# Performance work log

Hardware: AMD Instinct MI355X
Metric: run time of the kernel (lower is better)

Reference implementation:

```python
import jax, jax.numpy as jnp
import numpy as np

B, M, HID = 4, 4096, 1024
H, HD = 16, 64          # num_heads, head_dim
SEG = 128               # segment_size
DIL = 2                 # dilation_rate
SCALE = HD ** -0.5


def _hilbert_perm(n_side):
    """Linear indices (y*n+x) visited along a Hilbert curve on an n_side x n_side grid."""
    def d2xy(n, d):
        x = y = 0
        t = d
        s = 1
        while s < n:
            rx = 1 & (t // 2)
            ry = 1 & (t ^ rx)
            if ry == 0:
                if rx == 1:
                    x = s - 1 - x
                    y = s - 1 - y
                x, y = y, x
            x += s * rx
            y += s * ry
            t //= 4
            s *= 2
        return x, y
    idx = np.empty(n_side * n_side, dtype=np.int32)
    for d in range(n_side * n_side):
        x, y = d2xy(n_side, d)
        idx[d] = y * n_side + x
    return idx


def setup_inputs() -> dict:
    key = jax.random.key(0)
    k1, k2, k3 = jax.random.split(key, 3)
    x = jax.random.normal(k1, (B, M, HID), dtype=jnp.float32)
    w_qkv = jax.random.normal(k2, (3 * HID, HID), dtype=jnp.float32) * 0.02
    w_out = jax.random.normal(k3, (HID, HID), dtype=jnp.float32) * 0.02
    hilbert_map = jnp.asarray(_hilbert_perm(int(np.sqrt(M))))  # permutation of [0, M)
    return {"x": x, "w_qkv": w_qkv, "w_out": w_out, "hilbert_map": hilbert_map}


def reference(x, w_qkv, w_out, hilbert_map):
    nseg = M // SEG
    # qkv projection (nn.Linear, no bias): [B, M, 3*HID]
    qkv = x @ w_qkv.T
    qkv = qkv.reshape(B, M, 3, H, HD).transpose(2, 0, 3, 1, 4)  # [3, B, H, M, HD]
    # Hilbert reorder along sequence dim
    qkv = qkv[:, :, :, hilbert_map, :]
    q, k, v = qkv[0], qkv[1], qkv[2]
    # segment into blocks of SEG: [B, H, nseg, SEG, HD]
    q = q.reshape(B, H, nseg, SEG, HD)
    k = k.reshape(B, H, nseg, SEG, HD)
    v = v.reshape(B, H, nseg, SEG, HD)
    scores = jnp.einsum("bhnsd,bhntd->bhnst", q, k) * SCALE
    # dilation mask: position is active if (pos % DIL == 0); pair allowed if row OR col active
    active = (jnp.arange(SEG) % DIL) == 0
    mask = active[:, None] | active[None, :]  # [SEG, SEG]
    scores = jnp.where(mask, scores, jnp.float32(-1e30))
    attn = jax.nn.softmax(scores, axis=-1)
    out = jnp.einsum("bhnst,bhntd->bhnsd", attn, v)  # [B, H, nseg, SEG, HD]
    # output stays in Hilbert order (matches custom autograd semantics)
    out = out.reshape(B, H, M, HD).transpose(0, 2, 1, 3).reshape(B, M, HID)
    return out @ w_out.T
```

## Files before the change

kernel.cpp:

```cpp
#include <hip/hip_runtime.h>
#include <stdint.h>


typedef __attribute__((ext_vector_type(8))) short short8;
typedef __attribute__((ext_vector_type(4))) short short4v;
typedef __attribute__((ext_vector_type(4))) float f32x4;

#define DEV __device__ __forceinline__

DEV short f2bf(float f) {
  union { float f; uint32_t u; } x; x.f = f;
  uint32_t r = x.u + 0x7fffu + ((x.u >> 16) & 1u);
  return (short)(r >> 16);
}

DEV void gload_lds16(const void* g, void* l) {
  __builtin_amdgcn_global_load_lds(
      (const __attribute__((address_space(1))) uint32_t*)g,
      (__attribute__((address_space(3))) uint32_t*)l, 16, 0, 0);
}

__global__ __launch_bounds__(256) void k_gather_cast(
    const float* __restrict__ x, const int* __restrict__ perm, short* __restrict__ xp) {
  const int row = blockIdx.x;
  const int b = row >> 12, pos = row & 4095;
  const int src = (b << 12) + perm[pos];
  const f32x4 v = ((const f32x4*)(x + (size_t)src * 1024))[threadIdx.x];
  short4v o = { f2bf(v[0]), f2bf(v[1]), f2bf(v[2]), f2bf(v[3]) };
  ((short4v*)(xp + (size_t)row * 1024))[threadIdx.x] = o;
}

__global__ __launch_bounds__(256) void k_cast(
    const float* __restrict__ src, short* __restrict__ dst) {
  const int i = blockIdx.x * 256 + threadIdx.x;
  const f32x4 v = ((const f32x4*)src)[i];
  short4v o = { f2bf(v[0]), f2bf(v[1]), f2bf(v[2]), f2bf(v[3]) };
  ((short4v*)dst)[i] = o;
}

template <int EPI>
__global__ __launch_bounds__(256, 3) void k_gemm(
    const short* __restrict__ A, const short* __restrict__ W,
    void* __restrict__ Cout, const int K, const int N) {
  __shared__ __attribute__((aligned(16))) short As[128 * 64];
  __shared__ __attribute__((aligned(16))) short Bs[128 * 64];
  const int tid = threadIdx.x;
  const int bi = blockIdx.y, bj = blockIdx.x;
  const int lane = tid & 63, w = tid >> 6;
  const int wr = w >> 1, wc = w & 1;
  const int lrow = lane & 15, lg = lane >> 4;

  f32x4 acc[4][4] = {};
  const size_t arow0 = (size_t)bi * 128;
  const size_t brow0 = (size_t)bj * 128;

  for (int k0 = 0; k0 < K; k0 += 64) {
    __syncthreads();
#pragma unroll
    for (int i = 0; i < 4; ++i) {
      int c = i * 256 + tid;
      int row = c >> 3, ch = c & 7;
      int g = ch ^ (row & 7);
      gload_lds16(A + (arow0 + row) * K + k0 + g * 8, &As[c * 8]);
      gload_lds16(W + (brow0 + row) * K + k0 + g * 8, &Bs[c * 8]);
    }
    __syncthreads();
#pragma unroll
    for (int kk = 0; kk < 2; ++kk) {
      short8 af[4], bfr[4];
#pragma unroll
      for (int mi = 0; mi < 4; ++mi) {
        int r = wr * 64 + mi * 16 + lrow;
        int pc = (kk * 4 + lg) ^ (r & 7);
        af[mi] = *(const short8*)&As[r * 64 + pc * 8];
      }
#pragma unroll
      for (int ni = 0; ni < 4; ++ni) {
        int r = wc * 64 + ni * 16 + lrow;
        int pc = (kk * 4 + lg) ^ (r & 7);
        bfr[ni] = *(const short8*)&Bs[r * 64 + pc * 8];
      }
#pragma unroll
      for (int mi = 0; mi < 4; ++mi)
#pragma unroll
        for (int ni = 0; ni < 4; ++ni)
          acc[mi][ni] = __builtin_amdgcn_mfma_f32_16x16x32_bf16(
              af[mi], bfr[ni], acc[mi][ni], 0, 0, 0);
    }
  }

  const int gr_base = bi * 128 + wr * 64;
  const int gc_base = bj * 128 + wc * 64;
  if (EPI == 0) {
    short* Q = (short*)Cout;
#pragma unroll
    for (int mi = 0; mi < 4; ++mi) {
#pragma unroll
      for (int reg = 0; reg < 4; ++reg) {
        int gr = gr_base + mi * 16 + 4 * lg + reg;
        int b = gr >> 12, pos = gr & 4095;
#pragma unroll
        for (int ni = 0; ni < 4; ++ni) {
          int gc = gc_base + ni * 16 + lrow;
          int sel = gc >> 10, h = (gc >> 6) & 15, d = gc & 63;
          size_t idx = ((((size_t)sel * 4 + b) * 16 + h) * 4096 + pos) * 64 + d;
          Q[idx] = f2bf(acc[mi][ni][reg]);
        }
      }
    }
  } else {
    float* C = (float*)Cout;
#pragma unroll
    for (int mi = 0; mi < 4; ++mi)
#pragma unroll
      for (int reg = 0; reg < 4; ++reg) {
        int gr = gr_base + mi * 16 + 4 * lg + reg;
#pragma unroll
        for (int ni = 0; ni < 4; ++ni) {
          int gc = gc_base + ni * 16 + lrow;
          C[(size_t)gr * N + gc] = acc[mi][ni][reg];
        }
      }
  }
}

__global__ __launch_bounds__(256, 2) void k_attn(
    const short* __restrict__ qkv, short* __restrict__ aout) {
  __shared__ __attribute__((aligned(16))) short Qs[128 * 64];
  __shared__ __attribute__((aligned(16))) short Ks[128 * 64];
  __shared__ __attribute__((aligned(16))) short Vt[64 * 128];
  __shared__ __attribute__((aligned(16))) short Ps[128 * 128];
  const int bid = blockIdx.x;
  const int seg = bid & 31, h = (bid >> 5) & 15, b = bid >> 9;
  const size_t plane = (size_t)4096 * 64;
  const short* qp = qkv + ((size_t)(0 * 4 + b) * 16 + h) * plane + seg * 128 * 64;
  const short* kp = qkv + ((size_t)(1 * 4 + b) * 16 + h) * plane + seg * 128 * 64;
  const short* vp = qkv + ((size_t)(2 * 4 + b) * 16 + h) * plane + seg * 128 * 64;
  const int tid = threadIdx.x, lane = tid & 63, w = tid >> 6;
  const int lrow = lane & 15, lg = lane >> 4;

#pragma unroll
  for (int i = 0; i < 4; ++i) {
    int c = i * 256 + tid;
    int row = c >> 3, ch = c & 7, g = ch ^ (row & 7);
    gload_lds16(qp + row * 64 + g * 8, &Qs[c * 8]);
    gload_lds16(kp + row * 64 + g * 8, &Ks[c * 8]);
  }
#pragma unroll
  for (int i = 0; i < 4; ++i) {
    int c = i * 256 + tid;
    int t = c >> 3, d0 = (c & 7) * 8;
    short8 v = *(const short8*)(vp + t * 64 + d0);
#pragma unroll
    for (int j = 0; j < 8; ++j) {
      int d = d0 + j;
      Vt[d * 128 + (t ^ ((d & 7) * 8))] = v[j];
    }
  }
  __syncthreads();

  f32x4 s[2][8] = {};
#pragma unroll
  for (int kk = 0; kk < 2; ++kk) {
    short8 qa[2];
#pragma unroll
    for (int mi = 0; mi < 2; ++mi) {
      int r = w * 32 + mi * 16 + lrow;
      int pc = (kk * 4 + lg) ^ (r & 7);
      qa[mi] = *(const short8*)&Qs[r * 64 + pc * 8];
    }
#pragma unroll
    for (int ni = 0; ni < 8; ++ni) {
      int r = ni * 16 + lrow;
      int pc = (kk * 4 + lg) ^ (r & 7);
      short8 kb = *(const short8*)&Ks[r * 64 + pc * 8];
#pragma unroll
      for (int mi = 0; mi < 2; ++mi)
        s[mi][ni] = __builtin_amdgcn_mfma_f32_16x16x32_bf16(qa[mi], kb, s[mi][ni], 0, 0, 0);
    }
  }

  float inv[2][4];
  const int oddcol = lane & 1;
#pragma unroll
  for (int mi = 0; mi < 2; ++mi) {
#pragma unroll
    for (int reg = 0; reg < 4; ++reg) {
      float pm = -3.0e38f;
#pragma unroll
      for (int ni = 0; ni < 8; ++ni) {
        float v = s[mi][ni][reg] * 0.125f;
        if ((reg & 1) && oddcol) v = -1.0e30f;
        s[mi][ni][reg] = v;
        pm = fmaxf(pm, v);
      }
#pragma unroll
      for (int off = 1; off < 16; off <<= 1) pm = fmaxf(pm, __shfl_xor(pm, off));
      float sum = 0.f;
#pragma unroll
      for (int ni = 0; ni < 8; ++ni) {
        float p = __expf(s[mi][ni][reg] - pm);
        s[mi][ni][reg] = p;
        sum += p;
      }
#pragma unroll
      for (int off = 1; off < 16; off <<= 1) sum += __shfl_xor(sum, off);
      inv[mi][reg] = 1.0f / sum;
    }
  }

#pragma unroll
  for (int mi = 0; mi < 2; ++mi)
#pragma unroll
    for (int ni = 0; ni < 8; ++ni)
#pragma unroll
      for (int reg = 0; reg < 4; ++reg) {
        int r = w * 32 + mi * 16 + 4 * lg + reg;
        int col = ni * 16 + lrow;
        Ps[r * 128 + (col ^ ((r & 7) * 8))] = f2bf(s[mi][ni][reg]);
      }

  f32x4 o[2][4] = {};
#pragma unroll
  for (int kt = 0; kt < 4; ++kt) {
    short8 pa[2];
#pragma unroll
    for (int mi = 0; mi < 2; ++mi) {
      int r = w * 32 + mi * 16 + lrow;
      int pc = (kt * 4 + lg) ^ (r & 7);
      pa[mi] = *(const short8*)&Ps[r * 128 + pc * 8];
    }
#pragma unroll
    for (int dn = 0; dn < 4; ++dn) {
      int d = dn * 16 + lrow;
      int pc = (kt * 4 + lg) ^ (d & 7);
      short8 vb = *(const short8*)&Vt[d * 128 + pc * 8];
#pragma unroll
      for (int mi = 0; mi < 2; ++mi)
        o[mi][dn] = __builtin_amdgcn_mfma_f32_16x16x32_bf16(pa[mi], vb, o[mi][dn], 0, 0, 0);
    }
  }

#pragma unroll
  for (int mi = 0; mi < 2; ++mi)
#pragma unroll
    for (int dn = 0; dn < 4; ++dn)
#pragma unroll
      for (int reg = 0; reg < 4; ++reg) {
        int r = w * 32 + mi * 16 + 4 * lg + reg;
        int pos = seg * 128 + r;
        int d = dn * 16 + lrow;
        aout[((size_t)(b * 4096 + pos)) * 1024 + h * 64 + d] =
            f2bf(o[mi][dn][reg] * inv[mi][reg]);
      }
}

extern "C" void kernel_launch(void* const* d_in, const int* in_sizes, int n_in,
                              void* d_out, int out_size, void* d_ws, size_t ws_size,
                              hipStream_t stream) {
  const float* x     = (const float*)d_in[0];
  const float* w_qkv = (const float*)d_in[1];
  const float* w_out = (const float*)d_in[2];
  const int*   perm  = (const int*)d_in[3];

  char* ws = (char*)d_ws;
  short* xp   = (short*)(ws);
  short* wq   = (short*)(ws + 33554432);
  short* wo   = (short*)(ws + 33554432 + 6291456);
  short* qkvb = (short*)(ws + 41943040);
  short* aout = xp;

  k_gather_cast<<<16384, 256, 0, stream>>>(x, perm, xp);
  k_cast<<<3072, 256, 0, stream>>>(w_qkv, wq);
  k_cast<<<1024, 256, 0, stream>>>(w_out, wo);
  k_gemm<0><<<dim3(24, 128), 256, 0, stream>>>(xp, wq, qkvb, 1024, 3072);
  k_attn<<<2048, 256, 0, stream>>>(qkvb, aout);
  k_gemm<1><<<dim3(8, 128), 256, 0, stream>>>(aout, wo, d_out, 1024, 1024);
}
```

Before: 322.4 us.

## Rewrite GEMMs as 256x256 8-wave double-buffered pipelined kernels; alias attention LDS

```diff
diff --git a/kernel.cpp b/kernel.cpp
--- a/kernel.cpp
+++ b/kernel.cpp
@@ -19,6 +19,11 @@
       (const __attribute__((address_space(1))) uint32_t*)g,
       (__attribute__((address_space(3))) uint32_t*)l, 16, 0, 0);
 }
+
+#define BAR() __builtin_amdgcn_s_barrier()
+#define LGKM0() do { asm volatile("s_waitcnt lgkmcnt(0)" ::: "memory"); \
+                     __builtin_amdgcn_sched_barrier(0); } while (0)
+#define VMC(n) asm volatile("s_waitcnt vmcnt(" #n ")" ::: "memory")
 
 __global__ __launch_bounds__(256) void k_gather_cast(
     const float* __restrict__ x, const int* __restrict__ perm, short* __restrict__ xp) {
@@ -38,98 +43,143 @@
   ((short4v*)dst)[i] = o;
 }
 
-template <int EPI>
-__global__ __launch_bounds__(256, 3) void k_gemm(
-    const short* __restrict__ A, const short* __restrict__ W,
-    void* __restrict__ Cout, const int K, const int N) {
-  __shared__ __attribute__((aligned(16))) short As[128 * 64];
-  __shared__ __attribute__((aligned(16))) short Bs[128 * 64];
+template <int EPI, int NBJ>
+__global__ __launch_bounds__(512, 2) void k_gemm8(
+    const short* __restrict__ A, const short* __restrict__ W, void* __restrict__ Cout) {
+  __shared__ __attribute__((aligned(16))) short lds[65536];
   const int tid = threadIdx.x;
-  const int bi = blockIdx.y, bj = blockIdx.x;
   const int lane = tid & 63, w = tid >> 6;
-  const int wr = w >> 1, wc = w & 1;
+  const int wr = w >> 2, wc = w & 3;
   const int lrow = lane & 15, lg = lane >> 4;
 
-  f32x4 acc[4][4] = {};
-  const size_t arow0 = (size_t)bi * 128;
-  const size_t brow0 = (size_t)bj * 128;
-
-  for (int k0 = 0; k0 < K; k0 += 64) {
-    __syncthreads();
-#pragma unroll
-    for (int i = 0; i < 4; ++i) {
-      int c = i * 256 + tid;
-      int row = c >> 3, ch = c & 7;
-      int g = ch ^ (row & 7);
-      gload_lds16(A + (arow0 + row) * K + k0 + g * 8, &As[c * 8]);
-      gload_lds16(W + (brow0 + row) * K + k0 + g * 8, &Bs[c * 8]);
-    }
-    __syncthreads();
-#pragma unroll
-    for (int kk = 0; kk < 2; ++kk) {
-      short8 af[4], bfr[4];
-#pragma unroll
-      for (int mi = 0; mi < 4; ++mi) {
-        int r = wr * 64 + mi * 16 + lrow;
-        int pc = (kk * 4 + lg) ^ (r & 7);
-        af[mi] = *(const short8*)&As[r * 64 + pc * 8];
-      }
-#pragma unroll
-      for (int ni = 0; ni < 4; ++ni) {
-        int r = wc * 64 + ni * 16 + lrow;
-        int pc = (kk * 4 + lg) ^ (r & 7);
-        bfr[ni] = *(const short8*)&Bs[r * 64 + pc * 8];
-      }
-#pragma unroll
-      for (int mi = 0; mi < 4; ++mi)
-#pragma unroll
-        for (int ni = 0; ni < 4; ++ni)
-          acc[mi][ni] = __builtin_amdgcn_mfma_f32_16x16x32_bf16(
-              af[mi], bfr[ni], acc[mi][ni], 0, 0, 0);
-    }
-  }
-
-  const int gr_base = bi * 128 + wr * 64;
-  const int gc_base = bj * 128 + wc * 64;
+  const int nwg = NBJ * 64;
+  const int cpx = nwg >> 3;
+  const int bid = blockIdx.x;
+  const int sw = (bid & 7) * cpx + (bid >> 3);
+  const int bi = sw / NBJ, bj = sw % NBJ;
+
+  const short* Abase = A + (size_t)bi * 256 * 1024;
+  const short* Bbase = W + (size_t)bj * 256 * 1024;
+
+  const int c0 = tid, c1 = tid + 512;
+  const int sOff0 = (c0 >> 3) * 1024 + (((c0 & 7) ^ ((c0 >> 3) & 7)) * 8);
+  const int sOff1 = (c1 >> 3) * 1024 + (((c1 & 7) ^ ((c1 >> 3) & 7)) * 8);
+  const int pc0 = lg ^ (lrow & 7), pc1 = (4 + lg) ^ (lrow & 7);
+
+  f32x4 acc[2][4][2][2] = {};
+  short8 af[4][2], bfrag[2][2][2];
+
+#define ISSUE(base, half, tile, isB) do {                                   \
+    const short* _s = (base) + (half) * (128 * 1024) + (tile) * 64;         \
+    short* _d = lds + (((tile) & 1) * 32768) + (isB) * 16384 + (half) * 8192; \
+    gload_lds16(_s + sOff0, _d + c0 * 8);                                   \
+    gload_lds16(_s + sOff1, _d + c1 * 8);                                   \
+  } while (0)
+
+#define LDA(mh) do {                                                        \
+    const short* _b = ldsbuf + (mh) * 8192;                                 \
+    _Pragma("unroll") for (int mi = 0; mi < 4; ++mi) {                      \
+      const short* _r = _b + (wr * 64 + mi * 16 + lrow) * 64;               \
+      af[mi][0] = *(const short8*)(_r + pc0 * 8);                           \
+      af[mi][1] = *(const short8*)(_r + pc1 * 8); } } while (0)
+
+#define LDB(nh) do {                                                        \
+    const short* _b = ldsbuf + 16384 + (nh) * 8192;                         \
+    _Pragma("unroll") for (int ni = 0; ni < 2; ++ni) {                      \
+      const short* _r = _b + (wc * 32 + ni * 16 + lrow) * 64;               \
+      bfrag[nh][ni][0] = *(const short8*)(_r + pc0 * 8);                    \
+      bfrag[nh][ni][1] = *(const short8*)(_r + pc1 * 8); } } while (0)
+
+#define MM(mh, nh) do {                                                     \
+    _Pragma("unroll") for (int mi = 0; mi < 4; ++mi)                        \
+    _Pragma("unroll") for (int ni = 0; ni < 2; ++ni) {                      \
+      acc[mh][mi][nh][ni] = __builtin_amdgcn_mfma_f32_16x16x32_bf16(        \
+          af[mi][0], bfrag[nh][ni][0], acc[mh][mi][nh][ni], 0, 0, 0);       \
+      acc[mh][mi][nh][ni] = __builtin_amdgcn_mfma_f32_16x16x32_bf16(        \
+          af[mi][1], bfrag[nh][ni][1], acc[mh][mi][nh][ni], 0, 0, 0); } } while (0)
+
+  ISSUE(Abase, 0, 0, 0); ISSUE(Bbase, 0, 0, 1);
+  ISSUE(Abase, 1, 0, 0); ISSUE(Bbase, 1, 0, 1);
+  ISSUE(Abase, 0, 1, 0); ISSUE(Bbase, 0, 1, 1);
+  VMC(4);
+  BAR();
+
+#pragma unroll 2
+  for (int t = 0; t < 16; ++t) {
+    const short* ldsbuf = lds + ((t & 1) * 32768);
+    LDA(0); LDB(0);
+    if (t + 1 < 16) ISSUE(Abase, 1, t + 1, 0);
+    BAR(); LGKM0();
+    __builtin_amdgcn_s_setprio(1); MM(0, 0); __builtin_amdgcn_s_setprio(0);
+    BAR();
+    LDB(1);
+    if (t + 1 < 16) ISSUE(Bbase, 1, t + 1, 1);
+    BAR(); LGKM0();
+    __builtin_amdgcn_s_setprio(1); MM(0, 1); __builtin_amdgcn_s_setprio(0);
+    BAR();
+    LDA(1);
+    if (t + 2 < 16) ISSUE(Abase, 0, t + 2, 0);
+    BAR(); LGKM0();
+    __builtin_amdgcn_s_setprio(1); MM(1, 0); __builtin_amdgcn_s_setprio(0);
+    BAR();
+    if (t + 2 < 16) ISSUE(Bbase, 0, t + 2, 1);
+    BAR(); LGKM0();
+    __builtin_amdgcn_s_setprio(1); MM(1, 1); __builtin_amdgcn_s_setprio(0);
+    if (t + 2 < 16) { VMC(4); } else { VMC(0); }
+    BAR();
+  }
+#undef ISSUE
+#undef LDA
+#undef LDB
+#undef MM
+
   if (EPI == 0) {
     short* Q = (short*)Cout;
 #pragma unroll
-    for (int mi = 0; mi < 4; ++mi) {
-#pragma unroll
-      for (int reg = 0; reg < 4; ++reg) {
-        int gr = gr_base + mi * 16 + 4 * lg + reg;
-        int b = gr >> 12, pos = gr & 4095;
-#pragma unroll
-        for (int ni = 0; ni < 4; ++ni) {
-          int gc = gc_base + ni * 16 + lrow;
-          int sel = gc >> 10, h = (gc >> 6) & 15, d = gc & 63;
-          size_t idx = ((((size_t)sel * 4 + b) * 16 + h) * 4096 + pos) * 64 + d;
-          Q[idx] = f2bf(acc[mi][ni][reg]);
-        }
+    for (int mh = 0; mh < 2; ++mh)
+#pragma unroll
+    for (int mi = 0; mi < 4; ++mi)
+#pragma unroll
+    for (int reg = 0; reg < 4; ++reg) {
+      const int gr = bi * 256 + mh * 128 + wr * 64 + mi * 16 + 4 * lg + reg;
+      const int b = gr >> 12, pos = gr & 4095;
+#pragma unroll
+      for (int nh = 0; nh < 2; ++nh)
+#pragma unroll
+      for (int ni = 0; ni < 2; ++ni) {
+        const int gc = bj * 256 + nh * 128 + wc * 32 + ni * 16 + lrow;
+        const int sel = gc >> 10, h = (gc >> 6) & 15, d = gc & 63;
+        Q[((((size_t)sel * 4 + b) * 16 + h) * 4096 + pos) * 64 + d] =
+            f2bf(acc[mh][mi][nh][ni][reg]);
       }
     }
   } else {
     float* C = (float*)Cout;
 #pragma unroll
+    for (int mh = 0; mh < 2; ++mh)
+#pragma unroll
     for (int mi = 0; mi < 4; ++mi)
 #pragma unroll
-      for (int reg = 0; reg < 4; ++reg) {
-        int gr = gr_base + mi * 16 + 4 * lg + reg;
-#pragma unroll
-        for (int ni = 0; ni < 4; ++ni) {
-          int gc = gc_base + ni * 16 + lrow;
-          C[(size_t)gr * N + gc] = acc[mi][ni][reg];
-        }
-      }
-  }
-}
-
-__global__ __launch_bounds__(256, 2) void k_attn(
+    for (int reg = 0; reg < 4; ++reg) {
+      const int gr = bi * 256 + mh * 128 + wr * 64 + mi * 16 + 4 * lg + reg;
+#pragma unroll
+      for (int nh = 0; nh < 2; ++nh)
+#pragma unroll
+      for (int ni = 0; ni < 2; ++ni) {
+        const int gc = bj * 256 + nh * 128 + wc * 32 + ni * 16 + lrow;
+        C[(size_t)gr * 1024 + gc] = acc[mh][mi][nh][ni][reg];
+      }
+    }
+  }
+}
+
+__global__ __launch_bounds__(256, 3) void k_attn(
     const short* __restrict__ qkv, short* __restrict__ aout) {
-  __shared__ __attribute__((aligned(16))) short Qs[128 * 64];
-  __shared__ __attribute__((aligned(16))) short Ks[128 * 64];
-  __shared__ __attribute__((aligned(16))) short Vt[64 * 128];
-  __shared__ __attribute__((aligned(16))) short Ps[128 * 128];
+  __shared__ __attribute__((aligned(16))) short smem[24576];
+  short* Qs = smem;
+  short* Ks = smem + 8192;
+  short* Vt = smem + 16384;
+  short* Ps = smem;
   const int bid = blockIdx.x;
   const int seg = bid & 31, h = (bid >> 5) & 15, b = bid >> 9;
   const size_t plane = (size_t)4096 * 64;
@@ -160,6 +210,7 @@
   __syncthreads();
 
   f32x4 s[2][8] = {};
+  __builtin_amdgcn_s_setprio(1);
 #pragma unroll
   for (int kk = 0; kk < 2; ++kk) {
     short8 qa[2];
@@ -179,6 +230,7 @@
         s[mi][ni] = __builtin_amdgcn_mfma_f32_16x16x32_bf16(qa[mi], kb, s[mi][ni], 0, 0, 0);
     }
   }
+  __builtin_amdgcn_s_setprio(0);
 
   float inv[2][4];
   const int oddcol = lane & 1;
@@ -209,6 +261,8 @@
     }
   }
 
+  __syncthreads();
+
 #pragma unroll
   for (int mi = 0; mi < 2; ++mi)
 #pragma unroll
@@ -221,6 +275,7 @@
       }
 
   f32x4 o[2][4] = {};
+  __builtin_amdgcn_s_setprio(1);
 #pragma unroll
   for (int kt = 0; kt < 4; ++kt) {
     short8 pa[2];
@@ -240,6 +295,7 @@
         o[mi][dn] = __builtin_amdgcn_mfma_f32_16x16x32_bf16(pa[mi], vb, o[mi][dn], 0, 0, 0);
     }
   }
+  __builtin_amdgcn_s_setprio(0);
 
 #pragma unroll
   for (int mi = 0; mi < 2; ++mi)
@@ -273,7 +329,7 @@
   k_gather_cast<<<16384, 256, 0, stream>>>(x, perm, xp);
   k_cast<<<3072, 256, 0, stream>>>(w_qkv, wq);
   k_cast<<<1024, 256, 0, stream>>>(w_out, wo);
-  k_gemm<0><<<dim3(24, 128), 256, 0, stream>>>(xp, wq, qkvb, 1024, 3072);
+  k_gemm8<0, 12><<<768, 512, 0, stream>>>(xp, wq, qkvb);
   k_attn<<<2048, 256, 0, stream>>>(qkvb, aout);
-  k_gemm<1><<<dim3(8, 128), 256, 0, stream>>>(aout, wo, d_out, 1024, 1024);
-}
+  k_gemm8<1, 4><<<256, 512, 0, stream>>>(aout, wo, d_out);
+}
```

Result: faster. 308.9 us (-4.2%).
